# Performance work log

Hardware: AMD Instinct MI355X
Metric: run time of the kernel (lower is better)

The kernel has to match this reference:

```python
import jax, jax.numpy as jnp
import numpy as np

B, S, D, H, DK, DV, W = 2, 8192, 1024, 16, 64, 64, 128


def setup_inputs() -> dict:
    key = jax.random.key(0)
    ks = jax.random.split(key, 5)
    scale = 0.02
    x = jax.random.normal(ks[0], (B, S, D), jnp.float32)
    Wq = jax.random.normal(ks[1], (D, H * DK), jnp.float32) * scale
    Wk = jax.random.normal(ks[2], (D, H * DK), jnp.float32) * scale
    Wv = jax.random.normal(ks[3], (D, H * DV), jnp.float32) * scale
    Wo = jax.random.normal(ks[4], (H * DV, D), jnp.float32) * scale
    return {"x": x, "Wq": Wq, "Wk": Wk, "Wv": Wv, "Wo": Wo, "window_size": W}


def _sliding_window_attn(x, Wq, Wk, Wv, Wo, window_size):
    b, s, d = x.shape
    dk = Wq.shape[1] // H
    dv = Wv.shape[1] // H
    Bq = window_size            # block size == band half-width
    nb = s // Bq                # number of query blocks

    # projections -> [B, H, S, dh]
    q = (x @ Wq).reshape(b, s, H, dk).transpose(0, 2, 1, 3)
    k = (x @ Wk).reshape(b, s, H, dk).transpose(0, 2, 1, 3)
    v = (x @ Wv).reshape(b, s, H, dv).transpose(0, 2, 1, 3)

    qb = q.reshape(b, H, nb, Bq, dk)

    # pad keys/values by one block on each side, gather 3-block local context
    kpad = jnp.pad(k, ((0, 0), (0, 0), (Bq, Bq), (0, 0)))
    vpad = jnp.pad(v, ((0, 0), (0, 0), (Bq, Bq), (0, 0)))
    kb = kpad.reshape(b, H, nb + 2, Bq, dk)
    vb = vpad.reshape(b, H, nb + 2, Bq, dv)
    kctx = jnp.concatenate([kb[:, :, :-2], kb[:, :, 1:-1], kb[:, :, 2:]], axis=3)  # [B,H,nb,3Bq,dk]
    vctx = jnp.concatenate([vb[:, :, :-2], vb[:, :, 1:-1], vb[:, :, 2:]], axis=3)  # [B,H,nb,3Bq,dv]

    scores = jnp.einsum("bhnqd,bhnkd->bhnqk", qb, kctx) / jnp.sqrt(jnp.asarray(dk, x.dtype))

    # banded mask: query global idx i = n*Bq + q_loc; key global idx j = (n-1)*Bq + k_loc
    q_loc = jnp.arange(Bq)[:, None]                 # [Bq,1]
    k_rel = jnp.arange(3 * Bq)[None, :] - Bq        # [1,3Bq], offset of j relative to block start
    band = jnp.abs(k_rel - q_loc) <= window_size    # [Bq,3Bq]
    j_global = jnp.arange(nb)[:, None, None] * Bq + k_rel[None]  # [nb,1,3Bq]
    valid = (j_global >= 0) & (j_global < s)
    mask = band[None] & valid                       # [nb,Bq,3Bq]

    neg = jnp.asarray(-1e9, scores.dtype)
    scores = jnp.where(mask[None, None], scores, neg)
    attn = jax.nn.softmax(scores, axis=-1)

    ctx = jnp.einsum("bhnqk,bhnkd->bhnqd", attn, vctx)           # [B,H,nb,Bq,dv]
    ctx = ctx.reshape(b, H, s, dv).transpose(0, 2, 1, 3).reshape(b, s, H * dv)
    return ctx @ Wo


def reference(x, Wq, Wk, Wv, Wo, window_size):
    return _sliding_window_attn(x, Wq, Wk, Wv, Wo, window_size)
```

## Files before the change

### kernel.cpp

```cpp
#include <hip/hip_runtime.h>


typedef __bf16 bf16_t;
typedef bf16_t bf16x8 __attribute__((ext_vector_type(8)));
typedef bf16_t bf16x4 __attribute__((ext_vector_type(4)));
typedef float f32x4 __attribute__((ext_vector_type(4)));

#define CEXP 0.18033688011112042f

__device__ __forceinline__ f32x4 mfma16(bf16x8 a, bf16x8 b, f32x4 c) {
  return __builtin_amdgcn_mfma_f32_16x16x32_bf16(a, b, c, 0, 0, 0);
}

#define GLL16(gptr, lptr)                                                     \
  __builtin_amdgcn_global_load_lds(                                           \
      (__attribute__((address_space(1))) void*)(gptr),                        \
      (__attribute__((address_space(3))) void*)(lptr), 16, 0, 0)

__global__ __launch_bounds__(256) void prep(const float* __restrict__ x,
                                            const float* __restrict__ W0,
                                            const float* __restrict__ W1,
                                            const float* __restrict__ W2,
                                            const float* __restrict__ W3,
                                            bf16_t* __restrict__ xb,
                                            bf16_t* T0, bf16_t* T1,
                                            bf16_t* T2, bf16_t* T3) {
  __shared__ float tile[32][33];
  const int t = threadIdx.x;
  if (blockIdx.x < 8192) {
    int i = blockIdx.x * 256 + t;
    f32x4 a = *(const f32x4*)&x[(size_t)i * 8];
    f32x4 b = *(const f32x4*)&x[(size_t)i * 8 + 4];
    bf16x8 o;
#pragma unroll
    for (int j = 0; j < 4; ++j) { o[j] = (bf16_t)a[j]; o[4 + j] = (bf16_t)b[j]; }
    *(bf16x8*)&xb[(size_t)i * 8] = o;
    return;
  }
  int wb = blockIdx.x - 8192;
  int z = wb >> 10, rem = wb & 1023;
  int bx = rem & 31, by = rem >> 5;
  const float* W; bf16_t* T;
  switch (z) {
    case 0: W = W0; T = T0; break;
    case 1: W = W1; T = T1; break;
    case 2: W = W2; T = T2; break;
    default: W = W3; T = T3; break;
  }
  int tx = t & 31, ty = t >> 5;
  int xc = bx * 32 + tx;
  int y0 = by * 32;
#pragma unroll
  for (int i = ty; i < 32; i += 8) tile[i][tx] = W[(size_t)(y0 + i) * 1024 + xc];
  __syncthreads();
  int xo = y0 + tx;
  int yo = bx * 32;
#pragma unroll
  for (int i = ty; i < 32; i += 8)
    T[(size_t)(yo + i) * 1024 + xo] = (bf16_t)tile[tx][i];
}

__global__ __launch_bounds__(256) void gemm_qkv(const bf16_t* __restrict__ A,
                                                const bf16_t* __restrict__ Bt,
                                                bf16_t* __restrict__ qh,
                                                bf16_t* __restrict__ kh,
                                                bf16_t* __restrict__ vT2) {
  __shared__ bf16_t As0[128 * 32];
  __shared__ bf16_t As1[128 * 32];
  __shared__ bf16_t Bs0[128 * 32];
  __shared__ bf16_t Bs1[128 * 32];
  const int t = threadIdx.x;
  const int K = 1024;
  const int id = blockIdx.y * 24 + blockIdx.x;
  const int swz = (id & 7) * 384 + (id >> 3);
  const int m0 = (swz / 24) << 7, n0 = (swz % 24) << 7;
  const int ar = t >> 2, ac = (t & 3) << 3;
  const bf16_t* Ag = A + (size_t)(m0 + ar) * K + ac;
  const bf16_t* Bg = Bt + (size_t)(n0 + ar) * K + ac;
  const size_t step64 = (size_t)64 * K;
  const int lane = t & 63;
  const int wm = ((t >> 7) & 1) << 6;
  const int wn = ((t >> 6) & 1) << 6;
  const int fr = lane & 15, quad = lane >> 4, fk = quad << 3;

  f32x4 acc[4][4] = {};
  for (int k0 = 0; k0 < K; k0 += 64) {
    GLL16(Ag + k0, &As0[ar * 32 + ac]);
    GLL16(Ag + step64 + k0, &As0[(ar + 64) * 32 + ac]);
    GLL16(Ag + k0 + 32, &As1[ar * 32 + ac]);
    GLL16(Ag + step64 + k0 + 32, &As1[(ar + 64) * 32 + ac]);
    GLL16(Bg + k0, &Bs0[ar * 32 + ac]);
    GLL16(Bg + step64 + k0, &Bs0[(ar + 64) * 32 + ac]);
    GLL16(Bg + k0 + 32, &Bs1[ar * 32 + ac]);
    GLL16(Bg + step64 + k0 + 32, &Bs1[(ar + 64) * 32 + ac]);
    __syncthreads();
#pragma unroll
    for (int hh = 0; hh < 2; ++hh) {
      const bf16_t* Asp = hh ? As1 : As0;
      const bf16_t* Bsp = hh ? Bs1 : Bs0;
      bf16x8 af[4], bfv[4];
#pragma unroll
      for (int i = 0; i < 4; ++i) af[i] = *(const bf16x8*)&Asp[(wm + i * 16 + fr) * 32 + fk];
#pragma unroll
      for (int j = 0; j < 4; ++j) bfv[j] = *(const bf16x8*)&Bsp[(wn + j * 16 + fr) * 32 + fk];
#pragma unroll
      for (int i = 0; i < 4; ++i)
#pragma unroll
        for (int j = 0; j < 4; ++j) acc[i][j] = mfma16(af[i], bfv[j], acc[i][j]);
    }
    __syncthreads();
  }

  const int colbase = n0 + wn;
  if (colbase < 2048) {
    bf16_t* dst = (colbase < 1024) ? qh : kh;
    const int cb = colbase & 1023;
#pragma unroll
    for (int i = 0; i < 4; ++i)
#pragma unroll
      for (int j = 0; j < 4; ++j) {
        int col = cb + j * 16 + fr;
        int h = col >> 6, dk = col & 63;
#pragma unroll
        for (int r = 0; r < 4; ++r) {
          int cm = m0 + wm + i * 16 + quad * 4 + r;
          int b = cm >> 13, s = cm & 8191;
          dst[((((size_t)(b * 16 + h) << 13) | s) << 6) | dk] = (bf16_t)acc[i][j][r];
        }
      }
  } else {
    const int cb = colbase - 2048;
#pragma unroll
    for (int i = 0; i < 4; ++i) {
      int s0 = m0 + wm + i * 16;
      int b = s0 >> 13, sblk = (s0 & 8191) >> 4;
#pragma unroll
      for (int j = 0; j < 4; ++j) {
        int col = cb + j * 16;
        int h = col >> 6, dv = (col & 63) + fr;
        bf16x4 pk;
#pragma unroll
        for (int r = 0; r < 4; ++r) pk[r] = (bf16_t)acc[i][j][r];
        *(bf16x4*)&vT2[((size_t)(b * 16 + h) * 512 + sblk) * 1024 + dv * 16 + quad * 4] = pk;
      }
    }
  }
}

__global__ __launch_bounds__(256) void gemm_bt(const bf16_t* __restrict__ A,
                                               const bf16_t* __restrict__ Bt,
                                               float* __restrict__ Cf,
                                               int M, int N, int K) {
  __shared__ bf16_t As0[128 * 32];
  __shared__ bf16_t As1[128 * 32];
  __shared__ bf16_t Bs0[128 * 32];
  __shared__ bf16_t Bs1[128 * 32];
  const int t = threadIdx.x;
  const int nx = gridDim.x;
  const int nwg = nx * gridDim.y;
  const int cpx = nwg >> 3;
  const int id = blockIdx.y * nx + blockIdx.x;
  const int swz = (id & 7) * cpx + (id >> 3);
  const int m0 = (swz / nx) << 7, n0 = (swz % nx) << 7;
  const int ar = t >> 2, ac = (t & 3) << 3;
  const bf16_t* Ag = A + (size_t)(m0 + ar) * K + ac;
  const bf16_t* Bg = Bt + (size_t)(n0 + ar) * K + ac;
  const size_t step64 = (size_t)64 * K;
  const int lane = t & 63;
  const int wm = ((t >> 7) & 1) << 6;
  const int wn = ((t >> 6) & 1) << 6;
  const int fr = lane & 15, fk = (lane >> 4) << 3;

  f32x4 acc[4][4] = {};
  for (int k0 = 0; k0 < K; k0 += 64) {
    GLL16(Ag + k0, &As0[ar * 32 + ac]);
    GLL16(Ag + step64 + k0, &As0[(ar + 64) * 32 + ac]);
    GLL16(Ag + k0 + 32, &As1[ar * 32 + ac]);
    GLL16(Ag + step64 + k0 + 32, &As1[(ar + 64) * 32 + ac]);
    GLL16(Bg + k0, &Bs0[ar * 32 + ac]);
    GLL16(Bg + step64 + k0, &Bs0[(ar + 64) * 32 + ac]);
    GLL16(Bg + k0 + 32, &Bs1[ar * 32 + ac]);
    GLL16(Bg + step64 + k0 + 32, &Bs1[(ar + 64) * 32 + ac]);
    __syncthreads();
#pragma unroll
    for (int hh = 0; hh < 2; ++hh) {
      const bf16_t* Asp = hh ? As1 : As0;
      const bf16_t* Bsp = hh ? Bs1 : Bs0;
      bf16x8 af[4], bfv[4];
#pragma unroll
      for (int i = 0; i < 4; ++i) af[i] = *(const bf16x8*)&Asp[(wm + i * 16 + fr) * 32 + fk];
#pragma unroll
      for (int j = 0; j < 4; ++j) bfv[j] = *(const bf16x8*)&Bsp[(wn + j * 16 + fr) * 32 + fk];
#pragma unroll
      for (int i = 0; i < 4; ++i)
#pragma unroll
        for (int j = 0; j < 4; ++j) acc[i][j] = mfma16(af[i], bfv[j], acc[i][j]);
    }
    __syncthreads();
  }
#pragma unroll
  for (int i = 0; i < 4; ++i)
#pragma unroll
    for (int j = 0; j < 4; ++j)
#pragma unroll
      for (int r = 0; r < 4; ++r) {
        int cm = m0 + wm + i * 16 + ((lane >> 4) << 2) + r;
        int cn = n0 + wn + j * 16 + fr;
        Cf[(size_t)cm * N + cn] = acc[i][j][r];
      }
}

#define SKK 72
#define SVS 136
#define PST 136

__global__ __launch_bounds__(256, 3) void swa(const bf16_t* __restrict__ qh,
                                              const bf16_t* __restrict__ kh,
                                              const bf16_t* __restrict__ vT2,
                                              bf16_t* __restrict__ ctx) {
  __shared__ bf16_t Ks[128 * SKK];
  __shared__ bf16_t Vs[64 * SVS];
  __shared__ bf16_t PsT[4][16 * PST];

  const int t = threadIdx.x, lane = t & 63, w = t >> 6;
  const int n = blockIdx.x, h = blockIdx.y, b = blockIdx.z;
  const int fr = lane & 15, quad = lane >> 4, fk = quad << 3;
  const size_t bh = (size_t)(b * 16 + h);

  bf16x8 aq[2][2];
  {
    const size_t qbase = (bh * 8192 + n * 128 + w * 32) * 64;
#pragma unroll
    for (int qt = 0; qt < 2; ++qt)
#pragma unroll
      for (int ks = 0; ks < 2; ++ks)
        aq[qt][ks] = *(const bf16x8*)&qh[qbase + (size_t)(qt * 16 + fr) * 64 + ks * 32 + fk];
  }

  bf16x8 kr[4], vr[4];
  auto loadKV = [&](int kn) {
#pragma unroll
    for (int it = 0; it < 4; ++it) {
      int c = it * 256 + t;
      kr[it] = *(const bf16x8*)&kh[(bh * 8192 + kn * 128 + (c >> 3)) * 64 + ((c & 7) << 3)];
      int sb = c >> 7, dv = (c & 127) >> 1, sh = c & 1;
      vr[it] = *(const bf16x8*)&vT2[(bh * 512 + kn * 8 + sb) * 1024 + dv * 16 + sh * 8];
    }
  };

  const int cbeg = (n == 0) ? 1 : 0;
  const int cend = (n == 63) ? 1 : 2;
  loadKV(n + cbeg - 1);

  float lrow[2] = {0.f, 0.f};
  f32x4 o[2][4] = {};

  for (int ch = cbeg; ch <= cend; ++ch) {
    __syncthreads();
#pragma unroll
    for (int it = 0; it < 4; ++it) {
      int c = it * 256 + t;
      *(bf16x8*)&Ks[(c >> 3) * SKK + ((c & 7) << 3)] = kr[it];
      int sb = c >> 7, dv = (c & 127) >> 1, sh = c & 1;
      *(bf16x8*)&Vs[dv * SVS + sb * 16 + sh * 8] = vr[it];
    }
    __syncthreads();
    if (ch < cend) loadKV(n + ch);

#pragma unroll
    for (int qt = 0; qt < 2; ++qt) {
      const int lo = (ch == 0) ? 2 * w + qt : 0;
      const int hi = (ch == 2) ? 2 * w + qt : 7;

      f32x4 st[8];
      __builtin_amdgcn_s_setprio(1);
#pragma unroll
      for (int kt = 0; kt < 8; ++kt) {
        if (kt < lo || kt > hi) continue;
        bf16x8 k0 = *(const bf16x8*)&Ks[(kt * 16 + fr) * SKK + fk];
        bf16x8 k1 = *(const bf16x8*)&Ks[(kt * 16 + fr) * SKK + 32 + fk];
        st[kt] = mfma16(k1, aq[qt][1], mfma16(k0, aq[qt][0], (f32x4){0.f, 0.f, 0.f, 0.f}));
      }
      __builtin_amdgcn_s_setprio(0);

#pragma unroll
      for (int kt = 0; kt < 8; ++kt) {
        if (kt < lo || kt > hi) continue;
        const bool dL = (ch == 0) && (kt == lo);
        const bool dR = (ch == 2) && (kt == hi);
        bf16x4 pk;
#pragma unroll
        for (int r = 0; r < 4; ++r) {
          float p = exp2f(st[kt][r] * CEXP);
          int kl = quad * 4 + r;
          if (dL) p = (kl >= fr) ? p : 0.f;
          if (dR) p = (kl <= fr) ? p : 0.f;
          lrow[qt] += p;
          pk[r] = (bf16_t)p;
        }
        *(bf16x4*)&PsT[w][fr * PST + kt * 16 + quad * 4] = pk;
      }
      if ((ch == 0) && (lo & 1)) {
        bf16x4 zz; zz[0] = zz[1] = zz[2] = zz[3] = (bf16_t)0.f;
        *(bf16x4*)&PsT[w][fr * PST + (lo - 1) * 16 + quad * 4] = zz;
      }
      if ((ch == 2) && !(hi & 1)) {
        bf16x4 zz; zz[0] = zz[1] = zz[2] = zz[3] = (bf16_t)0.f;
        *(bf16x4*)&PsT[w][fr * PST + (hi + 1) * 16 + quad * 4] = zz;
      }

      const int pl = lo >> 1, ph = hi >> 1;
      __builtin_amdgcn_s_setprio(1);
#pragma unroll
      for (int ks = 0; ks < 4; ++ks) {
        if (ks < pl || ks > ph) continue;
        bf16x8 pa = *(const bf16x8*)&PsT[w][fr * PST + ks * 32 + fk];
#pragma unroll
        for (int dt = 0; dt < 4; ++dt) {
          bf16x8 bv = *(const bf16x8*)&Vs[(dt * 16 + fr) * SVS + ks * 32 + fk];
          o[qt][dt] = mfma16(pa, bv, o[qt][dt]);
        }
      }
      __builtin_amdgcn_s_setprio(0);
    }
  }

#pragma unroll
  for (int qt = 0; qt < 2; ++qt) {
    lrow[qt] += __shfl_xor(lrow[qt], 16, 64);
    lrow[qt] += __shfl_xor(lrow[qt], 32, 64);
  }
  float ln[2][4];
#pragma unroll
  for (int qt = 0; qt < 2; ++qt)
#pragma unroll
    for (int r = 0; r < 4; ++r)
      ln[qt][r] = __shfl(lrow[qt], quad * 4 + r, 64);

#pragma unroll
  for (int qt = 0; qt < 2; ++qt)
#pragma unroll
    for (int dt = 0; dt < 4; ++dt)
#pragma unroll
      for (int r = 0; r < 4; ++r) {
        float ov = o[qt][dt][r] / ln[qt][r];
        int srow = n * 128 + w * 32 + qt * 16 + quad * 4 + r;
        ctx[((size_t)b * 8192 + srow) * 1024 + h * 64 + dt * 16 + fr] = (bf16_t)ov;
      }
}

extern "C" void kernel_launch(void* const* d_in, const int* in_sizes, int n_in,
                              void* d_out, int out_size, void* d_ws, size_t ws_size,
                              hipStream_t stream) {
  const float* x  = (const float*)d_in[0];
  const float* Wq = (const float*)d_in[1];
  const float* Wk = (const float*)d_in[2];
  const float* Wv = (const float*)d_in[3];
  const float* Wo = (const float*)d_in[4];
  float* out = (float*)d_out;

  char* p = (char*)d_ws;
  bf16_t* xb    = (bf16_t*)p; p += (size_t)16384 * 1024 * 2;
  bf16_t* WqkvT = (bf16_t*)p; p += (size_t)3 * 1024 * 1024 * 2;
  bf16_t* WoT   = (bf16_t*)p; p += (size_t)1024 * 1024 * 2;
  bf16_t* qhb   = (bf16_t*)p; p += (size_t)16384 * 1024 * 2;
  bf16_t* khb   = (bf16_t*)p; p += (size_t)16384 * 1024 * 2;
  bf16_t* vT2   = (bf16_t*)p; p += (size_t)16384 * 1024 * 2;
  bf16_t* ctx   = (bf16_t*)p; p += (size_t)16384 * 1024 * 2;

  prep<<<12288, 256, 0, stream>>>(x, Wq, Wk, Wv, Wo, xb, WqkvT,
                                  WqkvT + (size_t)1024 * 1024,
                                  WqkvT + (size_t)2 * 1024 * 1024, WoT);
  gemm_qkv<<<dim3(24, 128), 256, 0, stream>>>(xb, WqkvT, qhb, khb, vT2);
  swa<<<dim3(64, 16, 2), 256, 0, stream>>>(qhb, khb, vT2, ctx);
  gemm_bt<<<dim3(8, 128), 256, 0, stream>>>(ctx, WoT, out, 16384, 1024, 1024);
}
```

Before: 361.9 us.

## Use 256x256 GEMM tiles with 4-stage LDS ring pipeline and swizzle

Result: faster. 344.5 us (-4.8%).

```diff
diff --git a/kernel.cpp b/kernel.cpp
--- a/kernel.cpp
+++ b/kernel.cpp
@@ -60,70 +60,111 @@
     T[(size_t)(yo + i) * 1024 + xo] = (bf16_t)tile[tx][i];
 }
 
-__global__ __launch_bounds__(256) void gemm_qkv(const bf16_t* __restrict__ A,
-                                                const bf16_t* __restrict__ Bt,
-                                                bf16_t* __restrict__ qh,
-                                                bf16_t* __restrict__ kh,
-                                                bf16_t* __restrict__ vT2) {
-  __shared__ bf16_t As0[128 * 32];
-  __shared__ bf16_t As1[128 * 32];
-  __shared__ bf16_t Bs0[128 * 32];
-  __shared__ bf16_t Bs1[128 * 32];
-  const int t = threadIdx.x;
-  const int K = 1024;
-  const int id = blockIdx.y * 24 + blockIdx.x;
-  const int swz = (id & 7) * 384 + (id >> 3);
-  const int m0 = (swz / 24) << 7, n0 = (swz % 24) << 7;
-  const int ar = t >> 2, ac = (t & 3) << 3;
-  const bf16_t* Ag = A + (size_t)(m0 + ar) * K + ac;
-  const bf16_t* Bg = Bt + (size_t)(n0 + ar) * K + ac;
-  const size_t step64 = (size_t)64 * K;
-  const int lane = t & 63;
-  const int wm = ((t >> 7) & 1) << 6;
-  const int wn = ((t >> 6) & 1) << 6;
-  const int fr = lane & 15, quad = lane >> 4, fk = quad << 3;
-
-  f32x4 acc[4][4] = {};
-  for (int k0 = 0; k0 < K; k0 += 64) {
-    GLL16(Ag + k0, &As0[ar * 32 + ac]);
-    GLL16(Ag + step64 + k0, &As0[(ar + 64) * 32 + ac]);
-    GLL16(Ag + k0 + 32, &As1[ar * 32 + ac]);
-    GLL16(Ag + step64 + k0 + 32, &As1[(ar + 64) * 32 + ac]);
-    GLL16(Bg + k0, &Bs0[ar * 32 + ac]);
-    GLL16(Bg + step64 + k0, &Bs0[(ar + 64) * 32 + ac]);
-    GLL16(Bg + k0 + 32, &Bs1[ar * 32 + ac]);
-    GLL16(Bg + step64 + k0 + 32, &Bs1[(ar + 64) * 32 + ac]);
-    __syncthreads();
-#pragma unroll
-    for (int hh = 0; hh < 2; ++hh) {
-      const bf16_t* Asp = hh ? As1 : As0;
-      const bf16_t* Bsp = hh ? Bs1 : Bs0;
-      bf16x8 af[4], bfv[4];
-#pragma unroll
-      for (int i = 0; i < 4; ++i) af[i] = *(const bf16x8*)&Asp[(wm + i * 16 + fr) * 32 + fk];
-#pragma unroll
-      for (int j = 0; j < 4; ++j) bfv[j] = *(const bf16x8*)&Bsp[(wn + j * 16 + fr) * 32 + fk];
-#pragma unroll
-      for (int i = 0; i < 4; ++i)
-#pragma unroll
-        for (int j = 0; j < 4; ++j) acc[i][j] = mfma16(af[i], bfv[j], acc[i][j]);
-    }
-    __syncthreads();
-  }
-
-  const int colbase = n0 + wn;
+__device__ __forceinline__ void gemm256_loop(const bf16_t* __restrict__ A,
+                                             const bf16_t* __restrict__ Bt,
+                                             int m0, int n0,
+                                             bf16_t (*As)[8192],
+                                             bf16_t (*Bs)[8192],
+                                             f32x4 acc[8][4]) {
+  const int K = 1024, NT = 32;
+  const int t = threadIdx.x, l = t & 63, w = t >> 6;
+  const int fr = l & 15, quad = l >> 4;
+  const int wm = w >> 2, wn = w & 3;
+  const int srow = w * 16 + (l >> 2);
+  const int scol = ((l & 3) ^ ((l >> 3) & 3)) << 3;
+  const bf16_t* Asrc = A + (size_t)(m0 + srow) * K + scol;
+  const bf16_t* Bsrc = Bt + (size_t)(n0 + srow) * K + scol;
+  const size_t cstep = (size_t)128 * K;
+  const int sdst = w * 512 + l * 8;
+  const int rdoff = fr * 32 + ((quad ^ ((fr >> 1) & 3)) << 3);
+  const int abase = wm * 4096 + rdoff;
+  const int bbase = wn * 2048 + rdoff;
+
+#pragma unroll
+  for (int tt = 0; tt < 2; ++tt) {
+    GLL16(Asrc + tt * 32, &As[tt][sdst]);
+    GLL16(Asrc + cstep + tt * 32, &As[tt][4096 + sdst]);
+    GLL16(Bsrc + tt * 32, &Bs[tt][sdst]);
+    GLL16(Bsrc + cstep + tt * 32, &Bs[tt][4096 + sdst]);
+  }
+  asm volatile("s_waitcnt vmcnt(4)" ::: "memory");
+  __builtin_amdgcn_s_barrier();
+
+  for (int tk = 0; tk < NT; ++tk) {
+    const int slot = tk & 3;
+    const bf16_t* Ap = As[slot];
+    const bf16_t* Bp = Bs[slot];
+    const bool st = (tk + 2 < NT);
+    const int s2 = (tk + 2) & 3;
+    __builtin_amdgcn_sched_barrier(0);
+    bf16x8 bq[4], af[4];
+#pragma unroll
+    for (int j = 0; j < 4; ++j) bq[j] = *(const bf16x8*)&Bp[bbase + j * 512];
+#pragma unroll
+    for (int i = 0; i < 4; ++i) af[i] = *(const bf16x8*)&Ap[abase + i * 512];
+    if (st) {
+      GLL16(Asrc + (tk + 2) * 32, &As[s2][sdst]);
+      GLL16(Asrc + cstep + (tk + 2) * 32, &As[s2][4096 + sdst]);
+    }
+    __builtin_amdgcn_s_barrier();
+    __builtin_amdgcn_s_setprio(1);
+#pragma unroll
+    for (int i = 0; i < 4; ++i)
+#pragma unroll
+      for (int j = 0; j < 4; ++j) acc[i][j] = mfma16(af[i], bq[j], acc[i][j]);
+    __builtin_amdgcn_s_setprio(0);
+    __builtin_amdgcn_s_barrier();
+    __builtin_amdgcn_sched_barrier(0);
+#pragma unroll
+    for (int i = 0; i < 4; ++i) af[i] = *(const bf16x8*)&Ap[abase + (4 + i) * 512];
+    if (st) {
+      GLL16(Bsrc + (tk + 2) * 32, &Bs[s2][sdst]);
+      GLL16(Bsrc + cstep + (tk + 2) * 32, &Bs[s2][4096 + sdst]);
+      asm volatile("s_waitcnt vmcnt(4)" ::: "memory");
+    } else {
+      asm volatile("s_waitcnt vmcnt(0)" ::: "memory");
+    }
+    __builtin_amdgcn_s_barrier();
+    __builtin_amdgcn_s_setprio(1);
+#pragma unroll
+    for (int i = 0; i < 4; ++i)
+#pragma unroll
+      for (int j = 0; j < 4; ++j) acc[4 + i][j] = mfma16(af[i], bq[j], acc[4 + i][j]);
+    __builtin_amdgcn_s_setprio(0);
+    __builtin_amdgcn_s_barrier();
+  }
+}
+
+__global__ __launch_bounds__(512, 2) void gemm_qkv(const bf16_t* __restrict__ A,
+                                                   const bf16_t* __restrict__ Bt,
+                                                   bf16_t* __restrict__ qh,
+                                                   bf16_t* __restrict__ kh,
+                                                   bf16_t* __restrict__ vT2) {
+  __shared__ bf16_t As[4][8192];
+  __shared__ bf16_t Bs[4][8192];
+  const int id = blockIdx.y * 12 + blockIdx.x;
+  const int swz = (id & 7) * 96 + (id >> 3);
+  const int m0 = (swz / 12) << 8, n0 = (swz % 12) << 8;
+
+  f32x4 acc[8][4] = {};
+  gemm256_loop(A, Bt, m0, n0, As, Bs, acc);
+
+  const int t = threadIdx.x, l = t & 63, w = t >> 6;
+  const int fr = l & 15, quad = l >> 4;
+  const int wm = w >> 2, wn = w & 3;
+  const int colbase = n0 + wn * 64;
   if (colbase < 2048) {
     bf16_t* dst = (colbase < 1024) ? qh : kh;
     const int cb = colbase & 1023;
 #pragma unroll
-    for (int i = 0; i < 4; ++i)
+    for (int i = 0; i < 8; ++i)
 #pragma unroll
       for (int j = 0; j < 4; ++j) {
         int col = cb + j * 16 + fr;
         int h = col >> 6, dk = col & 63;
 #pragma unroll
         for (int r = 0; r < 4; ++r) {
-          int cm = m0 + wm + i * 16 + quad * 4 + r;
+          int cm = m0 + wm * 128 + i * 16 + quad * 4 + r;
           int b = cm >> 13, s = cm & 8191;
           dst[((((size_t)(b * 16 + h) << 13) | s) << 6) | dk] = (bf16_t)acc[i][j][r];
         }
@@ -131,8 +172,8 @@
   } else {
     const int cb = colbase - 2048;
 #pragma unroll
-    for (int i = 0; i < 4; ++i) {
-      int s0 = m0 + wm + i * 16;
+    for (int i = 0; i < 8; ++i) {
+      int s0 = m0 + wm * 128 + i * 16;
       int b = s0 >> 13, sblk = (s0 & 8191) >> 4;
 #pragma unroll
       for (int j = 0; j < 4; ++j) {
@@ -147,66 +188,30 @@
   }
 }
 
-__global__ __launch_bounds__(256) void gemm_bt(const bf16_t* __restrict__ A,
-                                               const bf16_t* __restrict__ Bt,
-                                               float* __restrict__ Cf,
-                                               int M, int N, int K) {
-  __shared__ bf16_t As0[128 * 32];
-  __shared__ bf16_t As1[128 * 32];
-  __shared__ bf16_t Bs0[128 * 32];
-  __shared__ bf16_t Bs1[128 * 32];
-  const int t = threadIdx.x;
-  const int nx = gridDim.x;
-  const int nwg = nx * gridDim.y;
-  const int cpx = nwg >> 3;
-  const int id = blockIdx.y * nx + blockIdx.x;
-  const int swz = (id & 7) * cpx + (id >> 3);
-  const int m0 = (swz / nx) << 7, n0 = (swz % nx) << 7;
-  const int ar = t >> 2, ac = (t & 3) << 3;
-  const bf16_t* Ag = A + (size_t)(m0 + ar) * K + ac;
-  const bf16_t* Bg = Bt + (size_t)(n0 + ar) * K + ac;
-  const size_t step64 = (size_t)64 * K;
-  const int lane = t & 63;
-  const int wm = ((t >> 7) & 1) << 6;
-  const int wn = ((t >> 6) & 1) << 6;
-  const int fr = lane & 15, fk = (lane >> 4) << 3;
-
-  f32x4 acc[4][4] = {};
-  for (int k0 = 0; k0 < K; k0 += 64) {
-    GLL16(Ag + k0, &As0[ar * 32 + ac]);
-    GLL16(Ag + step64 + k0, &As0[(ar + 64) * 32 + ac]);
-    GLL16(Ag + k0 + 32, &As1[ar * 32 + ac]);
-    GLL16(Ag + step64 + k0 + 32, &As1[(ar + 64) * 32 + ac]);
-    GLL16(Bg + k0, &Bs0[ar * 32 + ac]);
-    GLL16(Bg + step64 + k0, &Bs0[(ar + 64) * 32 + ac]);
-    GLL16(Bg + k0 + 32, &Bs1[ar * 32 + ac]);
-    GLL16(Bg + step64 + k0 + 32, &Bs1[(ar + 64) * 32 + ac]);
-    __syncthreads();
-#pragma unroll
-    for (int hh = 0; hh < 2; ++hh) {
-      const bf16_t* Asp = hh ? As1 : As0;
-      const bf16_t* Bsp = hh ? Bs1 : Bs0;
-      bf16x8 af[4], bfv[4];
-#pragma unroll
-      for (int i = 0; i < 4; ++i) af[i] = *(const bf16x8*)&Asp[(wm + i * 16 + fr) * 32 + fk];
-#pragma unroll
-      for (int j = 0; j < 4; ++j) bfv[j] = *(const bf16x8*)&Bsp[(wn + j * 16 + fr) * 32 + fk];
-#pragma unroll
-      for (int i = 0; i < 4; ++i)
-#pragma unroll
-        for (int j = 0; j < 4; ++j) acc[i][j] = mfma16(af[i], bfv[j], acc[i][j]);
-    }
-    __syncthreads();
-  }
-#pragma unroll
-  for (int i = 0; i < 4; ++i)
+__global__ __launch_bounds__(512, 2) void gemm_bt(const bf16_t* __restrict__ A,
+                                                  const bf16_t* __restrict__ Bt,
+                                                  float* __restrict__ Cf) {
+  __shared__ bf16_t As[4][8192];
+  __shared__ bf16_t Bs[4][8192];
+  const int id = blockIdx.y * 4 + blockIdx.x;
+  const int swz = (id & 7) * 32 + (id >> 3);
+  const int m0 = (swz >> 2) << 8, n0 = (swz & 3) << 8;
+
+  f32x4 acc[8][4] = {};
+  gemm256_loop(A, Bt, m0, n0, As, Bs, acc);
+
+  const int t = threadIdx.x, l = t & 63, w = t >> 6;
+  const int fr = l & 15, quad = l >> 4;
+  const int wm = w >> 2, wn = w & 3;
+#pragma unroll
+  for (int i = 0; i < 8; ++i)
 #pragma unroll
     for (int j = 0; j < 4; ++j)
 #pragma unroll
       for (int r = 0; r < 4; ++r) {
-        int cm = m0 + wm + i * 16 + ((lane >> 4) << 2) + r;
-        int cn = n0 + wn + j * 16 + fr;
-        Cf[(size_t)cm * N + cn] = acc[i][j][r];
+        int cm = m0 + wm * 128 + i * 16 + quad * 4 + r;
+        int cn = n0 + wn * 64 + j * 16 + fr;
+        Cf[(size_t)cm * 1024 + cn] = acc[i][j][r];
       }
 }
 
@@ -371,7 +376,7 @@
   prep<<<12288, 256, 0, stream>>>(x, Wq, Wk, Wv, Wo, xb, WqkvT,
                                   WqkvT + (size_t)1024 * 1024,
                                   WqkvT + (size_t)2 * 1024 * 1024, WoT);
-  gemm_qkv<<<dim3(24, 128), 256, 0, stream>>>(xb, WqkvT, qhb, khb, vT2);
+  gemm_qkv<<<dim3(12, 64), 512, 0, stream>>>(xb, WqkvT, qhb, khb, vT2);
   swa<<<dim3(64, 16, 2), 256, 0, stream>>>(qhb, khb, vT2, ctx);
-  gemm_bt<<<dim3(8, 128), 256, 0, stream>>>(ctx, WoT, out, 16384, 1024, 1024);
-}
+  gemm_bt<<<dim3(4, 64), 512, 0, stream>>>(ctx, WoT, out);
+}
```
